# Kernel tuning notes

Hardware: AMD Instinct MI355X
Metric: run time of the kernel (lower is better)

Reference implementation:

```python
import jax, jax.numpy as jnp
import numpy as np

N = 100000
E = 1600000
H = 128
M = 256
L = 6
G = 512          # number of graphs in the batch
A = 95           # num_atom_types
EXTRA = 3        # input_dim - 1
EPS = 1e-5


def swish(x):
    return x * jax.nn.sigmoid(x)


def setup_inputs() -> dict:
    key = jax.random.key(0)
    ks = jax.random.split(key, 16)
    z = jax.random.randint(ks[0], (N, 1), 0, A).astype(jnp.float32)
    extra = jax.random.normal(ks[1], (N, EXTRA), dtype=jnp.float32)
    x = jnp.concatenate([z, extra], axis=1)                     # [N, 4]
    edge_index = jax.random.randint(ks[2], (2, E), 0, N)        # [2, E]
    batch = jnp.sort(jax.random.randint(ks[3], (N,), 0, G))     # [N]
    s = 0.02
    z_embed = jax.random.normal(ks[4], (A, H), dtype=jnp.float32) * s
    extra_w = jax.random.normal(ks[5], (H, EXTRA), dtype=jnp.float32) * (1.0 / np.sqrt(EXTRA))
    extra_b = jnp.zeros((H,), jnp.float32)
    conv_w = jax.random.normal(ks[6], (L, H, H), dtype=jnp.float32) * (1.0 / np.sqrt(H))
    conv_b = jnp.zeros((L, H), jnp.float32)
    gamma = jnp.ones((L, H), jnp.float32)
    beta = jnp.zeros((L, H), jnp.float32)
    mean_scale = jnp.ones((L, H), jnp.float32)
    mlp_w1 = jax.random.normal(ks[7], (L, M, H), dtype=jnp.float32) * (1.0 / np.sqrt(H))
    mlp_b1 = jnp.zeros((L, M), jnp.float32)
    mlp_w2 = jax.random.normal(ks[8], (L, H, M), dtype=jnp.float32) * (1.0 / np.sqrt(M))
    mlp_b2 = jnp.zeros((L, H), jnp.float32)
    return dict(x=x, edge_index=edge_index, batch=batch, z_embed=z_embed,
                extra_w=extra_w, extra_b=extra_b, conv_w=conv_w, conv_b=conv_b,
                gamma=gamma, beta=beta, mean_scale=mean_scale,
                mlp_w1=mlp_w1, mlp_b1=mlp_b1, mlp_w2=mlp_w2, mlp_b2=mlp_b2)


def gnn_forward(x, edge_index, batch, z_embed, extra_w, extra_b, conv_w, conv_b,
                gamma, beta, mean_scale, mlp_w1, mlp_b1, mlp_w2, mlp_b2):
    z = x[:, 0].astype(jnp.int32)
    h = z_embed[z] + x[:, 1:] @ extra_w.T + extra_b                 # [N, H]

    # GCN: add self loops, symmetric normalization (computed once; graph is static)
    loop = jnp.arange(N)
    src = jnp.concatenate([edge_index[0], loop])
    dst = jnp.concatenate([edge_index[1], loop])
    deg = jax.ops.segment_sum(jnp.ones_like(dst, jnp.float32), dst, num_segments=N)
    dinv = jnp.where(deg > 0, jax.lax.rsqrt(jnp.maximum(deg, 1.0)), 0.0)
    norm = (dinv[src] * dinv[dst])[:, None]                         # [E+N, 1]

    cnt = jax.ops.segment_sum(jnp.ones((N,), jnp.float32), batch, num_segments=G)[:, None]
    cnt = jnp.maximum(cnt, 1.0)

    for i in range(L):
        h_res = h
        # GCNConv
        xw = h @ conv_w[i].T
        agg = jax.ops.segment_sum(xw[src] * norm, dst, num_segments=N) + conv_b[i]
        # GraphNorm: gamma * (x - alpha*mean) / sqrt(var + eps) + beta, per graph
        mean = jax.ops.segment_sum(agg, batch, num_segments=G) / cnt   # [G, H]
        sub = agg - mean_scale[i] * mean[batch]
        var = jax.ops.segment_sum(sub * sub, batch, num_segments=G) / cnt
        hn = gamma[i] * sub * jax.lax.rsqrt(var[batch] + EPS) + beta[i]
        ha = swish(hn)
        # residual MLP
        h = swish(swish(ha @ mlp_w1[i].T + mlp_b1[i]) @ mlp_w2[i].T + mlp_b2[i]) + h_res
    return h


def reference(x, edge_index, batch, z_embed, extra_w, extra_b, conv_w, conv_b,
              gamma, beta, mean_scale, mlp_w1, mlp_b1, mlp_w2, mlp_b2):
    return gnn_forward(x, edge_index, batch, z_embed, extra_w, extra_b, conv_w, conv_b,
                       gamma, beta, mean_scale, mlp_w1, mlp_b1, mlp_w2, mlp_b2)
```

## Files before the change

kernel.cpp:

```cpp
#include <hip/hip_runtime.h>

#define NN 100000
#define EE 1600000
#define HH 128
#define MM 256
#define LL 6
#define GG 512
#define SCAN_NB ((NN + 1023) / 1024)

typedef __attribute__((ext_vector_type(8))) short short8;
typedef __attribute__((ext_vector_type(4))) float floatx4;

__device__ __forceinline__ float swishf(float v) {
    return v / (1.0f + __expf(-v));
}

__device__ __forceinline__ unsigned short f2bf(float f) {
    unsigned u = __builtin_bit_cast(unsigned, f);
    unsigned r = u + 0x7FFFu + ((u >> 16) & 1u);
    return (unsigned short)(r >> 16);
}

__device__ __forceinline__ float bf2f(unsigned short u) {
    return __builtin_bit_cast(float, (unsigned)u << 16);
}

__device__ __forceinline__ float2 bf2f2(unsigned u) {
    float2 r;
    r.x = __builtin_bit_cast(float, u << 16);
    r.y = __builtin_bit_cast(float, u & 0xFFFF0000u);
    return r;
}

__global__ void k_embed(const float* __restrict__ x, const float* __restrict__ z_embed,
                        const float* __restrict__ ew, const float* __restrict__ eb,
                        unsigned short* __restrict__ hb) {
    int idx = blockIdx.x * blockDim.x + threadIdx.x;
    if (idx >= NN * 32) return;
    int n = idx >> 5;
    int c0 = (idx & 31) << 2;
    const float* xr = x + (size_t)n * 4;
    int z = (int)xr[0];
    float x1 = xr[1], x2 = xr[2], x3 = xr[3];
    const float* ze = z_embed + (size_t)z * HH + c0;
    float o[4];
#pragma unroll
    for (int j = 0; j < 4; ++j) {
        int c = c0 + j;
        o[j] = ze[j] + x1 * ew[c * 3 + 0] + x2 * ew[c * 3 + 1] + x3 * ew[c * 3 + 2] + eb[c];
    }
    uint2 p;
    p.x = (unsigned)f2bf(o[0]) | ((unsigned)f2bf(o[1]) << 16);
    p.y = (unsigned)f2bf(o[2]) | ((unsigned)f2bf(o[3]) << 16);
    *(uint2*)(hb + (size_t)n * HH + c0) = p;
}

__global__ void k_f2bf3(const float* __restrict__ s1, unsigned short* __restrict__ d1, int n1,
                        const float* __restrict__ s2, unsigned short* __restrict__ d2, int n2,
                        const float* __restrict__ s3, unsigned short* __restrict__ d3, int n3) {
    int i = blockIdx.x * blockDim.x + threadIdx.x;
    if (i < n1) {
        d1[i] = f2bf(s1[i]);
    } else if (i < n1 + n2) {
        d2[i - n1] = f2bf(s2[i - n1]);
    } else if (i < n1 + n2 + n3) {
        d3[i - n1 - n2] = f2bf(s3[i - n1 - n2]);
    }
}

__global__ __launch_bounds__(256) void k_degree_p(const int* __restrict__ dst,
                                                  int* __restrict__ deg) {
    int part = blockIdx.x & 7;
    int blk = blockIdx.x >> 3;
    int nb = gridDim.x >> 3;
    int lo = (int)((long long)part * NN / 8);
    int hi = (int)((long long)(part + 1) * NN / 8);
    for (int e = blk * 256 + threadIdx.x; e < EE; e += nb * 256) {
        int d = dst[e];
        if (d >= lo && d < hi) atomicAdd(&deg[d], 1);
    }
}

__global__ void k_dinv(const int* __restrict__ deg, float* __restrict__ dinv) {
    int n = blockIdx.x * blockDim.x + threadIdx.x;
    if (n < NN) dinv[n] = rsqrtf((float)(deg[n] + 1));
}

__global__ void k_scan1(const int* __restrict__ deg, int* __restrict__ bsum) {
    __shared__ int sd[256];
    int t = threadIdx.x;
    int base = blockIdx.x * 1024 + t * 4;
    int s = 0;
#pragma unroll
    for (int j = 0; j < 4; ++j) {
        int i = base + j;
        if (i < NN) s += deg[i];
    }
    sd[t] = s;
    __syncthreads();
    for (int off = 128; off > 0; off >>= 1) {
        if (t < off) sd[t] += sd[t + off];
        __syncthreads();
    }
    if (t == 0) bsum[blockIdx.x] = sd[0];
}

__global__ void k_scan2(const int* __restrict__ bsum, int* __restrict__ boff) {
    __shared__ int sd[128];
    int t = threadIdx.x;
    int v = (t < SCAN_NB) ? bsum[t] : 0;
    sd[t] = v;
    __syncthreads();
    for (int off = 1; off < 128; off <<= 1) {
        int u = (t >= off) ? sd[t - off] : 0;
        __syncthreads();
        sd[t] += u;
        __syncthreads();
    }
    boff[t] = sd[t] - v;
}

__global__ void k_scan3(const int* __restrict__ deg, const int* __restrict__ boff,
                        int* __restrict__ rowptr) {
    __shared__ int sd[256];
    int t = threadIdx.x;
    int base = blockIdx.x * 1024 + t * 4;
    int v[4];
    int s = 0;
#pragma unroll
    for (int j = 0; j < 4; ++j) {
        int i = base + j;
        v[j] = (i < NN) ? deg[i] : 0;
        s += v[j];
    }
    sd[t] = s;
    __syncthreads();
    for (int off = 1; off < 256; off <<= 1) {
        int u = (t >= off) ? sd[t - off] : 0;
        __syncthreads();
        sd[t] += u;
        __syncthreads();
    }
    int run = boff[blockIdx.x] + sd[t] - s;
#pragma unroll
    for (int j = 0; j < 4; ++j) {
        int i = base + j;
        if (i < NN) rowptr[i] = run;
        if (i == NN - 1) rowptr[NN] = run + v[j];
        run += v[j];
    }
}

__global__ __launch_bounds__(256) void k_fill_p(const int* __restrict__ ei,
                                                const int* __restrict__ rowptr,
                                                int* __restrict__ cursor,
                                                int* __restrict__ col) {
    int part = blockIdx.x & 7;
    int blk = blockIdx.x >> 3;
    int nb = gridDim.x >> 3;
    int lo = (int)((long long)part * NN / 8);
    int hi = (int)((long long)(part + 1) * NN / 8);
    for (int e = blk * 256 + threadIdx.x; e < EE; e += nb * 256) {
        int d = ei[EE + e];
        if (d >= lo && d < hi) {
            int p = atomicAdd(&cursor[d], 1);
            col[rowptr[d] + p] = ei[e];
        }
    }
}

__global__ void k_gptr(const int* __restrict__ batch, int* __restrict__ gptr) {
    int n = blockIdx.x * blockDim.x + threadIdx.x;
    if (n >= NN) return;
    int b = batch[n];
    int pb = (n == 0) ? -1 : batch[n - 1];
    for (int g = pb + 1; g <= b; ++g) gptr[g] = n;
    if (n == NN - 1) {
        for (int g = b + 1; g <= GG; ++g) gptr[g] = NN;
    }
}

template <int EPI>
__global__ __launch_bounds__(256) void k_gemm_mfma(const unsigned short* __restrict__ A,
                                                   const unsigned short* __restrict__ B,
                                                   const float* __restrict__ bias,
                                                   const void* aux, float* Cf,
                                                   unsigned short* __restrict__ Cb, int K,
                                                   int Cout, int writeF) {
    __shared__ unsigned short As[128][72];
    __shared__ unsigned short Bs[128][72];
    const int tid = threadIdx.x;
    const int wave = tid >> 6;
    const int lane = tid & 63;
    const int quad = lane >> 4;
    const int l16 = lane & 15;
    const int wr = (wave & 1) << 6;
    const int wc = (wave >> 1) << 6;
    const int rowBase = blockIdx.x * 128;
    const int colBase = blockIdx.y * 128;

    floatx4 acc[4][4];
    const floatx4 zed = {0.f, 0.f, 0.f, 0.f};
#pragma unroll
    for (int i = 0; i < 4; ++i)
#pragma unroll
        for (int j = 0; j < 4; ++j) acc[i][j] = zed;

    const int srow = tid >> 3;
    const int skk = (tid & 7) << 3;

    for (int k0 = 0; k0 < K; k0 += 64) {
        __syncthreads();
#pragma unroll
        for (int p = 0; p < 4; ++p) {
            int rl = srow + (p << 5);
            int r = rowBase + rl;
            if (r >= NN) r = NN - 1;
            uint4 va = *(const uint4*)(A + (size_t)r * K + k0 + skk);
            *(uint4*)(&As[rl][skk]) = va;
            uint4 vb = *(const uint4*)(B + (size_t)(colBase + rl) * K + k0 + skk);
            *(uint4*)(&Bs[rl][skk]) = vb;
        }
        __syncthreads();
#pragma unroll
        for (int ks = 0; ks < 2; ++ks) {
            int koff = (ks << 5) + (quad << 3);
            short8 a[4], b[4];
#pragma unroll
            for (int i = 0; i < 4; ++i) a[i] = *(const short8*)(&As[wr + (i << 4) + l16][koff]);
#pragma unroll
            for (int j = 0; j < 4; ++j) b[j] = *(const short8*)(&Bs[wc + (j << 4) + l16][koff]);
#pragma unroll
            for (int i = 0; i < 4; ++i)
#pragma unroll
                for (int j = 0; j < 4; ++j)
                    acc[i][j] =
                        __builtin_amdgcn_mfma_f32_16x16x32_bf16(a[i], b[j], acc[i][j], 0, 0, 0);
        }
    }

    float bv[4];
    if (EPI >= 1) {
#pragma unroll
        for (int j = 0; j < 4; ++j) bv[j] = bias[colBase + wc + (j << 4) + l16];
    }
#pragma unroll
    for (int i = 0; i < 4; ++i) {
#pragma unroll
        for (int reg = 0; reg < 4; ++reg) {
            int r = rowBase + wr + (i << 4) + (quad << 2) + reg;
            if (r < NN) {
                if (EPI == 0) {
                    float dv = ((const float*)aux)[r];
#pragma unroll
                    for (int j = 0; j < 4; ++j) {
                        int c = colBase + wc + (j << 4) + l16;
                        Cb[(size_t)r * Cout + c] = f2bf(acc[i][j][reg] * dv);
                    }
                } else if (EPI == 1) {
#pragma unroll
                    for (int j = 0; j < 4; ++j) {
                        int c = colBase + wc + (j << 4) + l16;
                        Cb[(size_t)r * Cout + c] = f2bf(swishf(acc[i][j][reg] + bv[j]));
                    }
                } else {
                    const unsigned short* res = (const unsigned short*)aux;
#pragma unroll
                    for (int j = 0; j < 4; ++j) {
                        int c = colBase + wc + (j << 4) + l16;
                        float o = swishf(acc[i][j][reg] + bv[j]) + bf2f(res[(size_t)r * HH + c]);
                        Cb[(size_t)r * HH + c] = f2bf(o);
                        if (writeF) Cf[(size_t)r * HH + c] = o;
                    }
                }
            }
        }
    }
}

__global__ __launch_bounds__(256) void k_agg(const unsigned short* __restrict__ y,
                                             const int* __restrict__ rowptr,
                                             const int* __restrict__ col,
                                             const float* __restrict__ dinv,
                                             const float* __restrict__ cb,
                                             unsigned short* __restrict__ agg) {
    int w = threadIdx.x >> 6;
    int lane = threadIdx.x & 63;
    int d = blockIdx.x * 4 + w;
    if (d >= NN) return;
    int c = lane << 1;
    const unsigned* yv = (const unsigned*)y;
    float2 acc = bf2f2(yv[(size_t)d * 64 + lane]);
    int beg = rowptr[d];
    int end = rowptr[d + 1];
    int e = beg;
    for (; e + 7 < end; e += 8) {
        int s[8];
#pragma unroll
        for (int q = 0; q < 8; ++q) s[q] = col[e + q];
        float2 v[8];
#pragma unroll
        for (int q = 0; q < 8; ++q) v[q] = bf2f2(yv[(size_t)s[q] * 64 + lane]);
#pragma unroll
        for (int q = 0; q < 8; ++q) {
            acc.x += v[q].x;
            acc.y += v[q].y;
        }
    }
    for (; e < end; ++e) {
        float2 v0 = bf2f2(yv[(size_t)col[e] * 64 + lane]);
        acc.x += v0.x;
        acc.y += v0.y;
    }
    float dv = dinv[d];
    float ox = acc.x * dv + cb[c];
    float oy = acc.y * dv + cb[c + 1];
    unsigned pk = (unsigned)f2bf(ox) | ((unsigned)f2bf(oy) << 16);
    ((unsigned*)agg)[(size_t)d * 64 + lane] = pk;
}

__global__ __launch_bounds__(512) void k_stats(const unsigned short* __restrict__ agg,
                                               const int* __restrict__ gptr,
                                               const float* __restrict__ ms,
                                               float* __restrict__ gmean,
                                               float* __restrict__ grstd) {
    __shared__ float s1[512];
    __shared__ float s2[512];
    int g = blockIdx.x;
    int t = threadIdx.x;
    int c = t & 127;
    int part = t >> 7;
    int beg = gptr[g];
    int end = gptr[g + 1];
    float S1 = 0.f, S2 = 0.f;
    for (int n = beg + part; n < end; n += 4) {
        float v = bf2f(agg[(size_t)n * HH + c]);
        S1 += v;
        S2 += v * v;
    }
    s1[t] = S1;
    s2[t] = S2;
    __syncthreads();
    if (part == 0) {
        S1 = (s1[c] + s1[c + 128]) + (s1[c + 256] + s1[c + 384]);
        S2 = (s2[c] + s2[c + 128]) + (s2[c + 256] + s2[c + 384]);
        int cnt = end - beg;
        float inv = 1.0f / (float)(cnt > 0 ? cnt : 1);
        float m = S1 * inv;
        float msc = ms[c];
        float var = S2 * inv - msc * (2.0f - msc) * m * m;
        gmean[g * HH + c] = m;
        grstd[g * HH + c] = rsqrtf(var + 1e-5f);
    }
}

__global__ void k_normswish(const unsigned short* __restrict__ agg,
                            const int* __restrict__ batch, const float* __restrict__ gamma,
                            const float* __restrict__ beta, const float* __restrict__ ms,
                            const float* __restrict__ gmean, const float* __restrict__ grstd,
                            unsigned short* __restrict__ ha) {
    int idx = blockIdx.x * blockDim.x + threadIdx.x;
    if (idx >= NN * 32) return;
    int n = idx >> 5;
    int c0 = (idx & 31) << 2;
    int g = batch[n];
    uint2 ain = *(const uint2*)(agg + (size_t)n * HH + c0);
    float2 a01 = bf2f2(ain.x);
    float2 a23 = bf2f2(ain.y);
    float av[4] = {a01.x, a01.y, a23.x, a23.y};
    unsigned short o[4];
#pragma unroll
    for (int j = 0; j < 4; ++j) {
        int c = c0 + j;
        float sub = av[j] - ms[c] * gmean[g * HH + c];
        float hn = gamma[c] * sub * grstd[g * HH + c] + beta[c];
        o[j] = f2bf(swishf(hn));
    }
    uint2 p;
    p.x = (unsigned)o[0] | ((unsigned)o[1] << 16);
    p.y = (unsigned)o[2] | ((unsigned)o[3] << 16);
    *(uint2*)(ha + (size_t)n * HH + c0) = p;
}

extern "C" void kernel_launch(void* const* d_in, const int* in_sizes, int n_in,
                              void* d_out, int out_size, void* d_ws, size_t ws_size,
                              hipStream_t stream) {
    const float* x = (const float*)d_in[0];
    const int* ei = (const int*)d_in[1];
    const int* batch = (const int*)d_in[2];
    const float* z_embed = (const float*)d_in[3];
    const float* extra_w = (const float*)d_in[4];
    const float* extra_b = (const float*)d_in[5];
    const float* conv_w = (const float*)d_in[6];
    const float* conv_b = (const float*)d_in[7];
    const float* gamma = (const float*)d_in[8];
    const float* beta = (const float*)d_in[9];
    const float* mean_scale = (const float*)d_in[10];
    const float* mlp_w1 = (const float*)d_in[11];
    const float* mlp_b1 = (const float*)d_in[12];
    const float* mlp_w2 = (const float*)d_in[13];
    const float* mlp_b2 = (const float*)d_in[14];
    float* h_out = (float*)d_out;

    char* wsB = (char*)d_ws;
    size_t off = 0;
    auto alloc = [&](size_t bytes) -> void* {
        void* p = (void*)(wsB + off);
        off = (off + bytes + 255) & ~(size_t)255;
        return p;
    };
    float* dinv = (float*)alloc((size_t)NN * 4);
    int* deg = (int*)alloc((size_t)NN * 4);
    int* cursor = (int*)alloc((size_t)NN * 4);
    int* rowptr = (int*)alloc((size_t)(NN + 1) * 4);
    int* bsum = (int*)alloc(128 * 4);
    int* boff = (int*)alloc(128 * 4);
    int* col = (int*)alloc((size_t)EE * 4);
    int* gptr = (int*)alloc((size_t)(GG + 1) * 4);
    float* gmean = (float*)alloc((size_t)GG * HH * 4);
    float* grstd = (float*)alloc((size_t)GG * HH * 4);
    unsigned short* wb =
        (unsigned short*)alloc((size_t)(LL * (HH * HH + MM * HH + HH * MM)) * 2);
    unsigned short* cwb = wb;
    unsigned short* w1b = wb + (size_t)LL * HH * HH;
    unsigned short* w2b = w1b + (size_t)LL * MM * HH;
    unsigned short* hb = (unsigned short*)alloc((size_t)NN * HH * 2);
    unsigned short* ybuf = (unsigned short*)alloc((size_t)NN * HH * 2);
    unsigned short* tb = (unsigned short*)alloc((size_t)NN * MM * 2);
    unsigned short* aggb = tb;

    hipMemsetAsync(deg, 0, (size_t)NN * 4, stream);
    hipMemsetAsync(cursor, 0, (size_t)NN * 4, stream);

    k_embed<<<(NN * 32 + 255) / 256, 256, 0, stream>>>(x, z_embed, extra_w, extra_b, hb);
    {
        int n1 = LL * HH * HH, n2 = LL * MM * HH, n3 = LL * HH * MM;
        int nt = n1 + n2 + n3;
        k_f2bf3<<<(nt + 255) / 256, 256, 0, stream>>>(conv_w, cwb, n1, mlp_w1, w1b, n2,
                                                      mlp_w2, w2b, n3);
    }
    k_degree_p<<<1024, 256, 0, stream>>>(ei + EE, deg);
    k_dinv<<<(NN + 255) / 256, 256, 0, stream>>>(deg, dinv);
    k_scan1<<<SCAN_NB, 256, 0, stream>>>(deg, bsum);
    k_scan2<<<1, 128, 0, stream>>>(bsum, boff);
    k_scan3<<<SCAN_NB, 256, 0, stream>>>(deg, boff, rowptr);
    k_fill_p<<<1024, 256, 0, stream>>>(ei, rowptr, cursor, col);
    k_gptr<<<(NN + 255) / 256, 256, 0, stream>>>(batch, gptr);

    dim3 g1((NN + 127) / 128, 1);
    dim3 g2((NN + 127) / 128, 2);
    for (int i = 0; i < LL; ++i) {
        k_gemm_mfma<0><<<g1, 256, 0, stream>>>(hb, cwb + (size_t)i * HH * HH, nullptr, dinv,
                                               nullptr, ybuf, HH, HH, 0);
        k_agg<<<(NN + 3) / 4, 256, 0, stream>>>(ybuf, rowptr, col, dinv,
                                                conv_b + (size_t)i * HH, aggb);
        k_stats<<<GG, 512, 0, stream>>>(aggb, gptr, mean_scale + (size_t)i * HH, gmean, grstd);
        k_normswish<<<(NN * 32 + 255) / 256, 256, 0, stream>>>(
            aggb, batch, gamma + (size_t)i * HH, beta + (size_t)i * HH,
            mean_scale + (size_t)i * HH, gmean, grstd, ybuf);
        k_gemm_mfma<1><<<g2, 256, 0, stream>>>(ybuf, w1b + (size_t)i * MM * HH,
                                               mlp_b1 + (size_t)i * MM, nullptr, nullptr, tb,
                                               HH, MM, 0);
        k_gemm_mfma<2><<<g1, 256, 0, stream>>>(tb, w2b + (size_t)i * HH * MM,
                                               mlp_b2 + (size_t)i * HH, hb, h_out, hb, MM, HH,
                                               i == LL - 1 ? 1 : 0);
    }
}
```

Baseline: 1.429 ms.

## Store activations in column-blocked layout and split aggregation by channel slice

Activations are stored in a blocked layout of 16-channel slabs, each holding all nodes. The GEMMs drop LDS staging and load MFMA fragments straight from global memory. Aggregation, stats and norm kernels are split across 8 channel partitions, so each gather touches a 32-byte slab row and one partition's working set stays more cache-resident. The trade-off is loss of LDS reuse in the GEMMs and more uncoalesced 32-byte gathers.

```diff
diff --git a/kernel.cpp b/kernel.cpp
--- a/kernel.cpp
+++ b/kernel.cpp
@@ -30,6 +30,10 @@
     r.x = __builtin_bit_cast(float, u << 16);
     r.y = __builtin_bit_cast(float, u & 0xFFFF0000u);
     return r;
+}
+
+__device__ __forceinline__ size_t blkaddr(int c, int r) {
+    return ((size_t)(c >> 4) * NN + r) * 16 + (c & 15);
 }
 
 __global__ void k_embed(const float* __restrict__ x, const float* __restrict__ z_embed,
@@ -52,7 +56,7 @@
     uint2 p;
     p.x = (unsigned)f2bf(o[0]) | ((unsigned)f2bf(o[1]) << 16);
     p.y = (unsigned)f2bf(o[2]) | ((unsigned)f2bf(o[3]) << 16);
-    *(uint2*)(hb + (size_t)n * HH + c0) = p;
+    *(uint2*)(hb + blkaddr(c0, n)) = p;
 }
 
 __global__ void k_f2bf3(const float* __restrict__ s1, unsigned short* __restrict__ d1, int n1,
@@ -180,15 +184,12 @@
     }
 }
 
-template <int EPI>
-__global__ __launch_bounds__(256) void k_gemm_mfma(const unsigned short* __restrict__ A,
-                                                   const unsigned short* __restrict__ B,
-                                                   const float* __restrict__ bias,
-                                                   const void* aux, float* Cf,
-                                                   unsigned short* __restrict__ Cb, int K,
-                                                   int Cout, int writeF) {
-    __shared__ unsigned short As[128][72];
-    __shared__ unsigned short Bs[128][72];
+template <int K, int EPI>
+__global__ __launch_bounds__(256) void k_gemm_reg(const unsigned short* __restrict__ A,
+                                                  const unsigned short* __restrict__ B,
+                                                  const float* __restrict__ bias,
+                                                  const void* aux, float* Cf,
+                                                  unsigned short* __restrict__ Cb, int writeF) {
     const int tid = threadIdx.x;
     const int wave = tid >> 6;
     const int lane = tid & 63;
@@ -206,37 +207,30 @@
 #pragma unroll
         for (int j = 0; j < 4; ++j) acc[i][j] = zed;
 
-    const int srow = tid >> 3;
-    const int skk = (tid & 7) << 3;
-
-    for (int k0 = 0; k0 < K; k0 += 64) {
-        __syncthreads();
-#pragma unroll
-        for (int p = 0; p < 4; ++p) {
-            int rl = srow + (p << 5);
-            int r = rowBase + rl;
-            if (r >= NN) r = NN - 1;
-            uint4 va = *(const uint4*)(A + (size_t)r * K + k0 + skk);
-            *(uint4*)(&As[rl][skk]) = va;
-            uint4 vb = *(const uint4*)(B + (size_t)(colBase + rl) * K + k0 + skk);
-            *(uint4*)(&Bs[rl][skk]) = vb;
-        }
-        __syncthreads();
-#pragma unroll
-        for (int ks = 0; ks < 2; ++ks) {
-            int koff = (ks << 5) + (quad << 3);
-            short8 a[4], b[4];
-#pragma unroll
-            for (int i = 0; i < 4; ++i) a[i] = *(const short8*)(&As[wr + (i << 4) + l16][koff]);
-#pragma unroll
-            for (int j = 0; j < 4; ++j) b[j] = *(const short8*)(&Bs[wc + (j << 4) + l16][koff]);
-#pragma unroll
-            for (int i = 0; i < 4; ++i)
-#pragma unroll
-                for (int j = 0; j < 4; ++j)
-                    acc[i][j] =
-                        __builtin_amdgcn_mfma_f32_16x16x32_bf16(a[i], b[j], acc[i][j], 0, 0, 0);
-        }
+    int ar[4];
+#pragma unroll
+    for (int i = 0; i < 4; ++i) {
+        int r = rowBase + wr + (i << 4) + l16;
+        ar[i] = r < NN ? r : NN - 1;
+    }
+    const unsigned short* Bbase = B + (size_t)(colBase + wc + l16) * K;
+
+#pragma unroll 4
+    for (int kc = 0; kc < K; kc += 32) {
+        int k = kc + (quad << 3);
+        short8 a[4], b[4];
+#pragma unroll
+        for (int i = 0; i < 4; ++i)
+            a[i] = *(const short8*)(A + ((size_t)(k >> 4) * NN + ar[i]) * 16 + (k & 15));
+#pragma unroll
+        for (int j = 0; j < 4; ++j)
+            b[j] = *(const short8*)(Bbase + (size_t)(j << 4) * K + k);
+#pragma unroll
+        for (int i = 0; i < 4; ++i)
+#pragma unroll
+            for (int j = 0; j < 4; ++j)
+                acc[i][j] =
+                    __builtin_amdgcn_mfma_f32_16x16x32_bf16(a[i], b[j], acc[i][j], 0, 0, 0);
     }
 
     float bv[4];
@@ -255,21 +249,21 @@
 #pragma unroll
                     for (int j = 0; j < 4; ++j) {
                         int c = colBase + wc + (j << 4) + l16;
-                        Cb[(size_t)r * Cout + c] = f2bf(acc[i][j][reg] * dv);
+                        Cb[blkaddr(c, r)] = f2bf(acc[i][j][reg] * dv);
                     }
                 } else if (EPI == 1) {
 #pragma unroll
                     for (int j = 0; j < 4; ++j) {
                         int c = colBase + wc + (j << 4) + l16;
-                        Cb[(size_t)r * Cout + c] = f2bf(swishf(acc[i][j][reg] + bv[j]));
+                        Cb[blkaddr(c, r)] = f2bf(swishf(acc[i][j][reg] + bv[j]));
                     }
                 } else {
                     const unsigned short* res = (const unsigned short*)aux;
 #pragma unroll
                     for (int j = 0; j < 4; ++j) {
                         int c = colBase + wc + (j << 4) + l16;
-                        float o = swishf(acc[i][j][reg] + bv[j]) + bf2f(res[(size_t)r * HH + c]);
-                        Cb[(size_t)r * HH + c] = f2bf(o);
+                        float o = swishf(acc[i][j][reg] + bv[j]) + bf2f(res[blkaddr(c, r)]);
+                        Cb[blkaddr(c, r)] = f2bf(o);
                         if (writeF) Cf[(size_t)r * HH + c] = o;
                     }
                 }
@@ -284,102 +278,115 @@
                                              const float* __restrict__ dinv,
                                              const float* __restrict__ cb,
                                              unsigned short* __restrict__ agg) {
-    int w = threadIdx.x >> 6;
+    int p = blockIdx.x & 7;
+    int chunk = blockIdx.x >> 3;
+    int wave = threadIdx.x >> 6;
     int lane = threadIdx.x & 63;
-    int d = blockIdx.x * 4 + w;
+    int g8 = lane >> 3;
+    int sub = lane & 7;
+    int d = chunk * 32 + (wave << 3) + g8;
     if (d >= NN) return;
-    int c = lane << 1;
-    const unsigned* yv = (const unsigned*)y;
-    float2 acc = bf2f2(yv[(size_t)d * 64 + lane]);
+    const unsigned* ys = (const unsigned*)y + (size_t)p * NN * 8;
+    float2 acc = bf2f2(ys[(size_t)d * 8 + sub]);
     int beg = rowptr[d];
     int end = rowptr[d + 1];
     int e = beg;
-    for (; e + 7 < end; e += 8) {
-        int s[8];
-#pragma unroll
-        for (int q = 0; q < 8; ++q) s[q] = col[e + q];
-        float2 v[8];
-#pragma unroll
-        for (int q = 0; q < 8; ++q) v[q] = bf2f2(yv[(size_t)s[q] * 64 + lane]);
-#pragma unroll
-        for (int q = 0; q < 8; ++q) {
-            acc.x += v[q].x;
-            acc.y += v[q].y;
-        }
+    for (; e + 3 < end; e += 4) {
+        int s0 = col[e], s1 = col[e + 1], s2 = col[e + 2], s3 = col[e + 3];
+        float2 v0 = bf2f2(ys[(size_t)s0 * 8 + sub]);
+        float2 v1 = bf2f2(ys[(size_t)s1 * 8 + sub]);
+        float2 v2 = bf2f2(ys[(size_t)s2 * 8 + sub]);
+        float2 v3 = bf2f2(ys[(size_t)s3 * 8 + sub]);
+        acc.x += (v0.x + v1.x) + (v2.x + v3.x);
+        acc.y += (v0.y + v1.y) + (v2.y + v3.y);
     }
     for (; e < end; ++e) {
-        float2 v0 = bf2f2(yv[(size_t)col[e] * 64 + lane]);
+        float2 v0 = bf2f2(ys[(size_t)col[e] * 8 + sub]);
         acc.x += v0.x;
         acc.y += v0.y;
     }
     float dv = dinv[d];
+    int c = p * 16 + sub * 2;
     float ox = acc.x * dv + cb[c];
     float oy = acc.y * dv + cb[c + 1];
     unsigned pk = (unsigned)f2bf(ox) | ((unsigned)f2bf(oy) << 16);
-    ((unsigned*)agg)[(size_t)d * 64 + lane] = pk;
-}
-
-__global__ __launch_bounds__(512) void k_stats(const unsigned short* __restrict__ agg,
+    ((unsigned*)agg)[(size_t)p * NN * 8 + (size_t)d * 8 + sub] = pk;
+}
+
+__global__ __launch_bounds__(256) void k_stats(const unsigned short* __restrict__ agg,
                                                const int* __restrict__ gptr,
                                                const float* __restrict__ ms,
                                                float* __restrict__ gmean,
                                                float* __restrict__ grstd) {
-    __shared__ float s1[512];
-    __shared__ float s2[512];
-    int g = blockIdx.x;
+    __shared__ float s1[256];
+    __shared__ float s2[256];
+    int p = blockIdx.x & 7;
+    int g = blockIdx.x >> 3;
     int t = threadIdx.x;
-    int c = t & 127;
-    int part = t >> 7;
+    int cc = t & 15;
+    int pr = t >> 4;
     int beg = gptr[g];
     int end = gptr[g + 1];
+    const unsigned short* ap = agg + (size_t)p * NN * 16;
     float S1 = 0.f, S2 = 0.f;
-    for (int n = beg + part; n < end; n += 4) {
-        float v = bf2f(agg[(size_t)n * HH + c]);
+    for (int n = beg + pr; n < end; n += 16) {
+        float v = bf2f(ap[(size_t)n * 16 + cc]);
         S1 += v;
         S2 += v * v;
     }
     s1[t] = S1;
     s2[t] = S2;
     __syncthreads();
-    if (part == 0) {
-        S1 = (s1[c] + s1[c + 128]) + (s1[c + 256] + s1[c + 384]);
-        S2 = (s2[c] + s2[c + 128]) + (s2[c + 256] + s2[c + 384]);
+    if (t < 16) {
+        float T1 = 0.f, T2 = 0.f;
+#pragma unroll
+        for (int k = 0; k < 16; ++k) {
+            T1 += s1[k * 16 + t];
+            T2 += s2[k * 16 + t];
+        }
         int cnt = end - beg;
         float inv = 1.0f / (float)(cnt > 0 ? cnt : 1);
-        float m = S1 * inv;
+        float m = T1 * inv;
+        int c = p * 16 + t;
         float msc = ms[c];
-        float var = S2 * inv - msc * (2.0f - msc) * m * m;
+        float var = T2 * inv - msc * (2.0f - msc) * m * m;
         gmean[g * HH + c] = m;
         grstd[g * HH + c] = rsqrtf(var + 1e-5f);
     }
 }
 
-__global__ void k_normswish(const unsigned short* __restrict__ agg,
-                            const int* __restrict__ batch, const float* __restrict__ gamma,
-                            const float* __restrict__ beta, const float* __restrict__ ms,
-                            const float* __restrict__ gmean, const float* __restrict__ grstd,
-                            unsigned short* __restrict__ ha) {
-    int idx = blockIdx.x * blockDim.x + threadIdx.x;
-    if (idx >= NN * 32) return;
-    int n = idx >> 5;
-    int c0 = (idx & 31) << 2;
+__global__ __launch_bounds__(256) void k_normswish(const unsigned short* __restrict__ agg,
+                                                   const int* __restrict__ batch,
+                                                   const float* __restrict__ gamma,
+                                                   const float* __restrict__ beta,
+                                                   const float* __restrict__ ms,
+                                                   const float* __restrict__ gmean,
+                                                   const float* __restrict__ grstd,
+                                                   unsigned short* __restrict__ ha) {
+    int p = blockIdx.x & 7;
+    int chunk = blockIdx.x >> 3;
+    int t = threadIdx.x;
+    int n = chunk * 64 + (t >> 2);
+    if (n >= NN) return;
+    int cc0 = (t & 3) << 2;
     int g = batch[n];
-    uint2 ain = *(const uint2*)(agg + (size_t)n * HH + c0);
+    size_t base = (size_t)p * NN * 16 + (size_t)n * 16 + cc0;
+    uint2 ain = *(const uint2*)(agg + base);
     float2 a01 = bf2f2(ain.x);
     float2 a23 = bf2f2(ain.y);
     float av[4] = {a01.x, a01.y, a23.x, a23.y};
     unsigned short o[4];
 #pragma unroll
     for (int j = 0; j < 4; ++j) {
-        int c = c0 + j;
+        int c = p * 16 + cc0 + j;
         float sub = av[j] - ms[c] * gmean[g * HH + c];
         float hn = gamma[c] * sub * grstd[g * HH + c] + beta[c];
         o[j] = f2bf(swishf(hn));
     }
-    uint2 p;
-    p.x = (unsigned)o[0] | ((unsigned)o[1] << 16);
-    p.y = (unsigned)o[2] | ((unsigned)o[3] << 16);
-    *(uint2*)(ha + (size_t)n * HH + c0) = p;
+    uint2 pk;
+    pk.x = (unsigned)o[0] | ((unsigned)o[1] << 16);
+    pk.y = (unsigned)o[2] | ((unsigned)o[3] << 16);
+    *(uint2*)(ha + base) = pk;
 }
 
 extern "C" void kernel_launch(void* const* d_in, const int* in_sizes, int n_in,
@@ -449,20 +456,24 @@
 
     dim3 g1((NN + 127) / 128, 1);
     dim3 g2((NN + 127) / 128, 2);
+    int aggGrid = ((NN + 31) / 32) * 8;
+    int nsGrid = ((NN + 63) / 64) * 8;
     for (int i = 0; i < LL; ++i) {
-        k_gemm_mfma<0><<<g1, 256, 0, stream>>>(hb, cwb + (size_t)i * HH * HH, nullptr, dinv,
-                                               nullptr, ybuf, HH, HH, 0);
-        k_agg<<<(NN + 3) / 4, 256, 0, stream>>>(ybuf, rowptr, col, dinv,
-                                                conv_b + (size_t)i * HH, aggb);
-        k_stats<<<GG, 512, 0, stream>>>(aggb, gptr, mean_scale + (size_t)i * HH, gmean, grstd);
-        k_normswish<<<(NN * 32 + 255) / 256, 256, 0, stream>>>(
-            aggb, batch, gamma + (size_t)i * HH, beta + (size_t)i * HH,
-            mean_scale + (size_t)i * HH, gmean, grstd, ybuf);
-        k_gemm_mfma<1><<<g2, 256, 0, stream>>>(ybuf, w1b + (size_t)i * MM * HH,
-                                               mlp_b1 + (size_t)i * MM, nullptr, nullptr, tb,
-                                               HH, MM, 0);
-        k_gemm_mfma<2><<<g1, 256, 0, stream>>>(tb, w2b + (size_t)i * HH * MM,
-                                               mlp_b2 + (size_t)i * HH, hb, h_out, hb, MM, HH,
-                                               i == LL - 1 ? 1 : 0);
-    }
-}
+        k_gemm_reg<HH, 0><<<g1, 256, 0, stream>>>(hb, cwb + (size_t)i * HH * HH, nullptr,
+                                                  dinv, nullptr, ybuf, 0);
+        k_agg<<<aggGrid, 256, 0, stream>>>(ybuf, rowptr, col, dinv, conv_b + (size_t)i * HH,
+                                           aggb);
+        k_stats<<<GG * 8, 256, 0, stream>>>(aggb, gptr, mean_scale + (size_t)i * HH, gmean,
+                                            grstd);
+        k_normswish<<<nsGrid, 256, 0, stream>>>(aggb, batch, gamma + (size_t)i * HH,
+                                                beta + (size_t)i * HH,
+                                                mean_scale + (size_t)i * HH, gmean, grstd,
+                                                ybuf);
+        k_gemm_reg<HH, 1><<<g2, 256, 0, stream>>>(ybuf, w1b + (size_t)i * MM * HH,
+                                                  mlp_b1 + (size_t)i * MM, nullptr, nullptr,
+                                                  tb, 0);
+        k_gemm_reg<MM, 2><<<g1, 256, 0, stream>>>(tb, w2b + (size_t)i * HH * MM,
+                                                  mlp_b2 + (size_t)i * HH, hb, h_out, hb,
+                                                  i == LL - 1 ? 1 : 0);
+    }
+}
```

Result: slower. 1.703 ms (+19.1%).

## Stage whole weight tile in LDS, stream A from global, widen agg loads

Applied to the files above, without the earlier changes.

The GEMM is templated on K. It now loads the full 128xK weight tile into shared memory once and reads the A fragments directly from global memory into registers, which removes the per-k-step A staging and repeated barriers. The aggregation kernel changes from one 4-byte load per lane per edge to 16-byte loads, with four lane groups handling different edges and combining their results through cross-lane shuffles. In exchange, the GEMM reads A from global with a strided, uncoalesced pattern, and the shared-memory footprint grows for K=256.

```diff
diff --git a/kernel.cpp b/kernel.cpp
--- a/kernel.cpp
+++ b/kernel.cpp
@@ -180,15 +180,13 @@
     }
 }
 
-template <int EPI>
-__global__ __launch_bounds__(256) void k_gemm_mfma(const unsigned short* __restrict__ A,
-                                                   const unsigned short* __restrict__ B,
-                                                   const float* __restrict__ bias,
-                                                   const void* aux, float* Cf,
-                                                   unsigned short* __restrict__ Cb, int K,
-                                                   int Cout, int writeF) {
-    __shared__ unsigned short As[128][72];
-    __shared__ unsigned short Bs[128][72];
+template <int K, int EPI>
+__global__ __launch_bounds__(256) void k_gemm(const unsigned short* __restrict__ A,
+                                              const unsigned short* __restrict__ B,
+                                              const float* __restrict__ bias, const void* aux,
+                                              float* Cf, unsigned short* __restrict__ Cb,
+                                              int writeF) {
+    __shared__ unsigned short Bs[128][K + 8];
     const int tid = threadIdx.x;
     const int wave = tid >> 6;
     const int lane = tid & 63;
@@ -199,6 +197,13 @@
     const int rowBase = blockIdx.x * 128;
     const int colBase = blockIdx.y * 128;
 
+#pragma unroll
+    for (int i = tid; i < 128 * (K / 8); i += 256) {
+        int r = i / (K / 8);
+        int kk = (i % (K / 8)) * 8;
+        *(uint4*)(&Bs[r][kk]) = *(const uint4*)(B + (size_t)(colBase + r) * K + kk);
+    }
+
     floatx4 acc[4][4];
     const floatx4 zed = {0.f, 0.f, 0.f, 0.f};
 #pragma unroll
@@ -206,39 +211,32 @@
 #pragma unroll
         for (int j = 0; j < 4; ++j) acc[i][j] = zed;
 
-    const int srow = tid >> 3;
-    const int skk = (tid & 7) << 3;
-
-    for (int k0 = 0; k0 < K; k0 += 64) {
-        __syncthreads();
-#pragma unroll
-        for (int p = 0; p < 4; ++p) {
-            int rl = srow + (p << 5);
-            int r = rowBase + rl;
-            if (r >= NN) r = NN - 1;
-            uint4 va = *(const uint4*)(A + (size_t)r * K + k0 + skk);
-            *(uint4*)(&As[rl][skk]) = va;
-            uint4 vb = *(const uint4*)(B + (size_t)(colBase + rl) * K + k0 + skk);
-            *(uint4*)(&Bs[rl][skk]) = vb;
-        }
-        __syncthreads();
-#pragma unroll
-        for (int ks = 0; ks < 2; ++ks) {
-            int koff = (ks << 5) + (quad << 3);
-            short8 a[4], b[4];
-#pragma unroll
-            for (int i = 0; i < 4; ++i) a[i] = *(const short8*)(&As[wr + (i << 4) + l16][koff]);
-#pragma unroll
-            for (int j = 0; j < 4; ++j) b[j] = *(const short8*)(&Bs[wc + (j << 4) + l16][koff]);
-#pragma unroll
-            for (int i = 0; i < 4; ++i)
-#pragma unroll
-                for (int j = 0; j < 4; ++j)
-                    acc[i][j] =
-                        __builtin_amdgcn_mfma_f32_16x16x32_bf16(a[i], b[j], acc[i][j], 0, 0, 0);
-        }
-    }
-
+    int ar[4];
+#pragma unroll
+    for (int i = 0; i < 4; ++i) {
+        int r = rowBase + wr + (i << 4) + l16;
+        ar[i] = r < NN ? r : NN - 1;
+    }
+
+    __syncthreads();
+
+#pragma unroll
+    for (int ks = 0; ks < K / 32; ++ks) {
+        int k = (ks << 5) + (quad << 3);
+        short8 a[4], b[4];
+#pragma unroll
+        for (int i = 0; i < 4; ++i) a[i] = *(const short8*)(A + (size_t)ar[i] * K + k);
+#pragma unroll
+        for (int j = 0; j < 4; ++j) b[j] = *(const short8*)(&Bs[wc + (j << 4) + l16][k]);
+#pragma unroll
+        for (int i = 0; i < 4; ++i)
+#pragma unroll
+            for (int j = 0; j < 4; ++j)
+                acc[i][j] =
+                    __builtin_amdgcn_mfma_f32_16x16x32_bf16(a[i], b[j], acc[i][j], 0, 0, 0);
+    }
+
+    const int Cout = gridDim.y << 7;
     float bv[4];
     if (EPI >= 1) {
 #pragma unroll
@@ -288,35 +286,48 @@
     int lane = threadIdx.x & 63;
     int d = blockIdx.x * 4 + w;
     if (d >= NN) return;
-    int c = lane << 1;
-    const unsigned* yv = (const unsigned*)y;
-    float2 acc = bf2f2(yv[(size_t)d * 64 + lane]);
+    int grp = lane >> 4;
+    int l16 = lane & 15;
+    const uint4* yv = (const uint4*)y;
+    float acc[8];
+#pragma unroll
+    for (int j = 0; j < 8; ++j) acc[j] = 0.f;
+    if (grp == 0) {
+        uint4 v = yv[(size_t)d * 16 + l16];
+        float2 p0 = bf2f2(v.x), p1 = bf2f2(v.y), p2 = bf2f2(v.z), p3 = bf2f2(v.w);
+        acc[0] = p0.x; acc[1] = p0.y; acc[2] = p1.x; acc[3] = p1.y;
+        acc[4] = p2.x; acc[5] = p2.y; acc[6] = p3.x; acc[7] = p3.y;
+    }
     int beg = rowptr[d];
     int end = rowptr[d + 1];
-    int e = beg;
-    for (; e + 7 < end; e += 8) {
-        int s[8];
-#pragma unroll
-        for (int q = 0; q < 8; ++q) s[q] = col[e + q];
-        float2 v[8];
-#pragma unroll
-        for (int q = 0; q < 8; ++q) v[q] = bf2f2(yv[(size_t)s[q] * 64 + lane]);
-#pragma unroll
-        for (int q = 0; q < 8; ++q) {
-            acc.x += v[q].x;
-            acc.y += v[q].y;
-        }
-    }
-    for (; e < end; ++e) {
-        float2 v0 = bf2f2(yv[(size_t)col[e] * 64 + lane]);
-        acc.x += v0.x;
-        acc.y += v0.y;
-    }
-    float dv = dinv[d];
-    float ox = acc.x * dv + cb[c];
-    float oy = acc.y * dv + cb[c + 1];
-    unsigned pk = (unsigned)f2bf(ox) | ((unsigned)f2bf(oy) << 16);
-    ((unsigned*)agg)[(size_t)d * 64 + lane] = pk;
+    for (int e = beg + grp; e < end; e += 4) {
+        int s = col[e];
+        uint4 v = yv[(size_t)s * 16 + l16];
+        float2 p0 = bf2f2(v.x), p1 = bf2f2(v.y), p2 = bf2f2(v.z), p3 = bf2f2(v.w);
+        acc[0] += p0.x; acc[1] += p0.y; acc[2] += p1.x; acc[3] += p1.y;
+        acc[4] += p2.x; acc[5] += p2.y; acc[6] += p3.x; acc[7] += p3.y;
+    }
+#pragma unroll
+    for (int j = 0; j < 8; ++j) {
+        acc[j] += __shfl_xor(acc[j], 16, 64);
+        acc[j] += __shfl_xor(acc[j], 32, 64);
+    }
+    if (grp == 0) {
+        float dv = dinv[d];
+        float4 c0 = *(const float4*)(cb + l16 * 8);
+        float4 c1 = *(const float4*)(cb + l16 * 8 + 4);
+        float o[8];
+        o[0] = acc[0] * dv + c0.x; o[1] = acc[1] * dv + c0.y;
+        o[2] = acc[2] * dv + c0.z; o[3] = acc[3] * dv + c0.w;
+        o[4] = acc[4] * dv + c1.x; o[5] = acc[5] * dv + c1.y;
+        o[6] = acc[6] * dv + c1.z; o[7] = acc[7] * dv + c1.w;
+        uint4 pk;
+        pk.x = (unsigned)f2bf(o[0]) | ((unsigned)f2bf(o[1]) << 16);
+        pk.y = (unsigned)f2bf(o[2]) | ((unsigned)f2bf(o[3]) << 16);
+        pk.z = (unsigned)f2bf(o[4]) | ((unsigned)f2bf(o[5]) << 16);
+        pk.w = (unsigned)f2bf(o[6]) | ((unsigned)f2bf(o[7]) << 16);
+        *(uint4*)(agg + (size_t)d * HH + l16 * 8) = pk;
+    }
 }
 
 __global__ __launch_bounds__(512) void k_stats(const unsigned short* __restrict__ agg,
@@ -450,19 +461,18 @@
     dim3 g1((NN + 127) / 128, 1);
     dim3 g2((NN + 127) / 128, 2);
     for (int i = 0; i < LL; ++i) {
-        k_gemm_mfma<0><<<g1, 256, 0, stream>>>(hb, cwb + (size_t)i * HH * HH, nullptr, dinv,
-                                               nullptr, ybuf, HH, HH, 0);
+        k_gemm<HH, 0><<<g1, 256, 0, stream>>>(hb, cwb + (size_t)i * HH * HH, nullptr, dinv,
+                                              nullptr, ybuf, 0);
         k_agg<<<(NN + 3) / 4, 256, 0, stream>>>(ybuf, rowptr, col, dinv,
                                                 conv_b + (size_t)i * HH, aggb);
         k_stats<<<GG, 512, 0, stream>>>(aggb, gptr, mean_scale + (size_t)i * HH, gmean, grstd);
         k_normswish<<<(NN * 32 + 255) / 256, 256, 0, stream>>>(
             aggb, batch, gamma + (size_t)i * HH, beta + (size_t)i * HH,
             mean_scale + (size_t)i * HH, gmean, grstd, ybuf);
-        k_gemm_mfma<1><<<g2, 256, 0, stream>>>(ybuf, w1b + (size_t)i * MM * HH,
-                                               mlp_b1 + (size_t)i * MM, nullptr, nullptr, tb,
-                                               HH, MM, 0);
-        k_gemm_mfma<2><<<g1, 256, 0, stream>>>(tb, w2b + (size_t)i * HH * MM,
-                                               mlp_b2 + (size_t)i * HH, hb, h_out, hb, MM, HH,
-                                               i == LL - 1 ? 1 : 0);
-    }
-}
+        k_gemm<HH, 1><<<g2, 256, 0, stream>>>(ybuf, w1b + (size_t)i * MM * HH,
+                                              mlp_b1 + (size_t)i * MM, nullptr, nullptr, tb, 0);
+        k_gemm<MM, 2><<<g1, 256, 0, stream>>>(tb, w2b + (size_t)i * HH * MM,
+                                              mlp_b2 + (size_t)i * HH, hb, h_out, hb,
+                                              i == LL - 1 ? 1 : 0);
+    }
+}
```

Result: slower. 1.532 ms (+7.2%).
